# Kernel tuning notes

Measured on AMD Instinct MI355X. Metric: run time of the kernel, lower is better.

The kernel has to match this reference:

```python
import jax, jax.numpy as jnp
import numpy as np

NUM_ENT = 30000
NUM_ATTR_VALUES = 10000
NUM_NODES = NUM_ENT + NUM_ATTR_VALUES
NUM_REL = 230
NUM_ATTR_TYPES = 10
HIDDEN = 200          # num_bases=200 -> 1x1 block decomposition (per-rel diagonal)
N_EDGES = 600000
TIME_INTERVAL = 24
NUM_TIMESTAMPS = 365
PERIOD = 7
TRANX = 0.1
AMPY = 0.005
BATCH = 4096
RRELU_SLOPE = (1.0 / 8.0 + 1.0 / 3.0) / 2.0  # F.rrelu in eval mode


def setup_inputs() -> dict:
    key = jax.random.key(0)
    ks = jax.random.split(key, 12)
    ent_emb = jax.random.normal(ks[0], (NUM_ENT, HIDDEN), jnp.float32)            # nn.init.normal_
    attr_emb = jax.random.normal(ks[1], (NUM_ATTR_VALUES, HIDDEN), jnp.float32) * 0.05
    rel_emb = jax.random.normal(ks[2], (NUM_REL, HIDDEN), jnp.float32) * 0.1
    t = jnp.arange(NUM_TIMESTAMPS, dtype=jnp.float32)
    time_emb = (AMPY * (jnp.sin(2.0 * jnp.pi * t / PERIOD) + 1.0) + TRANX)[:, None]  # (T,1), frozen
    # RGCNBlockLayer weight: (num_rels, num_bases*submat_in*submat_out) = (10, 200)
    rgcn_weight = jax.random.normal(ks[3], (NUM_ATTR_TYPES, HIDDEN), jnp.float32) * 0.1
    dec_W = jax.random.normal(ks[4], (HIDDEN, 2 * HIDDEN + 1), jnp.float32) * 0.05
    dec_b = jnp.zeros((HIDDEN,), jnp.float32)
    edge_src = jax.random.randint(ks[5], (N_EDGES,), 0, NUM_NODES)
    edge_dst = jax.random.randint(ks[6], (N_EDGES,), 0, NUM_NODES)
    edge_type = jax.random.randint(ks[7], (N_EDGES,), 0, NUM_ATTR_TYPES)
    deg = jax.ops.segment_sum(jnp.ones((N_EDGES,), jnp.float32), edge_dst, num_segments=NUM_NODES)
    norm = (1.0 / jnp.clip(deg, 1.0))[:, None]  # (NUM_NODES, 1) in-degree norm
    ent_idx = jax.random.randint(ks[8], (BATCH,), 0, NUM_ENT)
    rel_idx = jax.random.randint(ks[9], (BATCH,), 0, NUM_REL)
    obj_idx = jax.random.randint(ks[10], (BATCH,), 0, NUM_ENT)
    time_raw = jax.random.randint(ks[11], (BATCH,), 0, NUM_TIMESTAMPS * TIME_INTERVAL)
    batch_data = jnp.stack([ent_idx, rel_idx, obj_idx, time_raw], axis=1)  # (B, 4)
    return {
        'ent_emb': ent_emb, 'attr_emb': attr_emb, 'rel_emb': rel_emb,
        'time_emb': time_emb, 'rgcn_weight': rgcn_weight,
        'dec_W': dec_W, 'dec_b': dec_b, 'norm': norm,
        'edge_src': edge_src, 'edge_dst': edge_dst, 'edge_type': edge_type,
        'batch_data': batch_data,
    }


def reference(ent_emb, attr_emb, rel_emb, time_emb, rgcn_weight, dec_W, dec_b,
              norm, edge_src, edge_dst, edge_type, batch_data):
    # --- RGCNBlockLayer (1x1 blocks): gather, per-relation diagonal multiply, scatter-sum ---
    h0 = jnp.concatenate([ent_emb, attr_emb], axis=0)           # (N, H)
    msg = h0[edge_src] * rgcn_weight[edge_type]                  # (E, H)
    agg = jax.ops.segment_sum(msg, edge_dst, num_segments=h0.shape[0])
    h = agg * norm                                               # apply_func: h * norm
    h = jnp.where(h >= 0, h, RRELU_SLOPE * h)                    # rrelu (eval); dropout=identity
    static_emb = h[:NUM_ENT]                                     # (num_ent, H)
    # --- embedding lookups ---
    ent = static_emb[batch_data[:, 0]]                           # (B, H)
    rel = rel_emb[batch_data[:, 1]]                              # (B, H)
    tim = time_emb[batch_data[:, 3] // TIME_INTERVAL]            # (B, 1)
    # --- decoder: tanh -> cat -> linear -> (dropout) -> relu -> mm ---
    x = jnp.concatenate([jnp.tanh(ent), rel, tim], axis=1)       # (B, 2H+1)
    x = x @ dec_W.T + dec_b                                      # (B, H)
    x = jax.nn.relu(x)
    return x @ static_emb.T                                      # (B, num_ent)
```

## Files before the change

### kernel.cpp

```cpp
#include <hip/hip_runtime.h>
#include <hip/hip_bf16.h>

#define NUM_ENT   30000
#define NUM_ATTR  10000
#define NUM_NODES 40000
#define NUM_TYPES 10
#define HIDDEN    200
#define KPAD      224
#define XP        416
#define NPAD      30080
#define N_EDGES   600000
#define BATCH     4096
#define XDIM      401
#define RRELU_SLOPE 0.22916666666666666f

using bf16x8 = __attribute__((ext_vector_type(8))) short;
using f32x4  = __attribute__((ext_vector_type(4))) float;
typedef __hip_bfloat16 bf16;

__device__ inline float bf2f(ushort u) { return __uint_as_float((unsigned)u << 16); }

__global__ void k_cvt(const float* __restrict__ ent, const float* __restrict__ attr,
                      ushort* __restrict__ h0b) {
    int i4 = blockIdx.x * blockDim.x + threadIdx.x;
    if (i4 >= NUM_NODES * HIDDEN / 4) return;
    int base = i4 * 4;
    const float* src = (base < NUM_ENT * HIDDEN) ? ent + base
                                                 : attr + (base - NUM_ENT * HIDDEN);
    float4 v = *reinterpret_cast<const float4*>(src);
    ushort4 o;
    o.x = __bfloat16_as_ushort(__float2bfloat16(v.x));
    o.y = __bfloat16_as_ushort(__float2bfloat16(v.y));
    o.z = __bfloat16_as_ushort(__float2bfloat16(v.z));
    o.w = __bfloat16_as_ushort(__float2bfloat16(v.w));
    *reinterpret_cast<ushort4*>(h0b + base) = o;
}

__global__ __launch_bounds__(1024) void k_prep(const float* __restrict__ norm,
                                               int* __restrict__ offsets,
                                               int* __restrict__ cursor) {
    __shared__ int part[1024];
    int t = threadIdx.x;
    const int CH = (NUM_ENT + 1023) / 1024;
    int base = t * CH;
    int caps[CH];
    int s = 0;
    for (int i = 0; i < CH; ++i) {
        int idx = base + i;
        int c = 0;
        if (idx < NUM_ENT) c = (int)(1.0f / norm[idx] + 0.5f);
        caps[i] = c;
        s += c;
    }
    part[t] = s;
    __syncthreads();
    for (int off = 1; off < 1024; off <<= 1) {
        int v = (t >= off) ? part[t - off] : 0;
        __syncthreads();
        part[t] += v;
        __syncthreads();
    }
    int run = (t == 0) ? 0 : part[t - 1];
    for (int i = 0; i < CH; ++i) {
        int idx = base + i;
        if (idx < NUM_ENT) {
            offsets[idx] = run;
            cursor[idx]  = run;
            run += caps[i];
        }
    }
}

__global__ void k_place(const int* __restrict__ edst, const int* __restrict__ esrc,
                        const int* __restrict__ etype, int* __restrict__ cursor,
                        int* __restrict__ sorted) {
    int e = blockIdx.x * blockDim.x + threadIdx.x;
    if (e < N_EDGES) {
        int d = edst[e];
        if (d < NUM_ENT) {
            int p = atomicAdd(&cursor[d], 1);
            sorted[p] = (esrc[e] << 4) | etype[e];
        }
    }
}

__global__ void k_aggregate(const ushort* __restrict__ h0b, const float* __restrict__ w,
                            const int* __restrict__ offsets, const int* __restrict__ cursor,
                            const int* __restrict__ sorted, const float* __restrict__ norm,
                            bf16* __restrict__ S) {
    __shared__ float wl[NUM_TYPES * HIDDEN];
    __shared__ float part[2][200];
    for (int i = threadIdx.x; i < NUM_TYPES * HIDDEN; i += blockDim.x)
        wl[i] = w[i];
    __syncthreads();

    int wid  = threadIdx.x >> 6;
    int lane = threadIdx.x & 63;
    int ln   = wid >> 1;
    int sub  = wid & 1;
    int n    = blockIdx.x * 2 + ln;
    bool live = (n < NUM_ENT);
    bool act  = lane < 50;
    int  c    = lane * 4;

    float4 a0 = make_float4(0, 0, 0, 0), a1 = a0, a2 = a0, a3 = a0;
    if (live) {
        int beg = offsets[n], end = cursor[n];
        int mid = beg + ((end - beg + 1) >> 1);
        int lo = sub ? mid : beg;
        int hi = sub ? end : mid;
        int e = lo;
        for (; e + 4 <= hi; e += 4) {
            int r0 = sorted[e + 0], r1 = sorted[e + 1], r2 = sorted[e + 2], r3 = sorted[e + 3];
            if (act) {
                ushort4 h0 = *reinterpret_cast<const ushort4*>(h0b + (size_t)(r0 >> 4) * HIDDEN + c);
                ushort4 h1 = *reinterpret_cast<const ushort4*>(h0b + (size_t)(r1 >> 4) * HIDDEN + c);
                ushort4 h2 = *reinterpret_cast<const ushort4*>(h0b + (size_t)(r2 >> 4) * HIDDEN + c);
                ushort4 h3 = *reinterpret_cast<const ushort4*>(h0b + (size_t)(r3 >> 4) * HIDDEN + c);
                const float* w0 = &wl[(r0 & 15) * HIDDEN + c];
                const float* w1 = &wl[(r1 & 15) * HIDDEN + c];
                const float* w2 = &wl[(r2 & 15) * HIDDEN + c];
                const float* w3 = &wl[(r3 & 15) * HIDDEN + c];
                a0.x += bf2f(h0.x) * w0[0]; a0.y += bf2f(h0.y) * w0[1];
                a0.z += bf2f(h0.z) * w0[2]; a0.w += bf2f(h0.w) * w0[3];
                a1.x += bf2f(h1.x) * w1[0]; a1.y += bf2f(h1.y) * w1[1];
                a1.z += bf2f(h1.z) * w1[2]; a1.w += bf2f(h1.w) * w1[3];
                a2.x += bf2f(h2.x) * w2[0]; a2.y += bf2f(h2.y) * w2[1];
                a2.z += bf2f(h2.z) * w2[2]; a2.w += bf2f(h2.w) * w2[3];
                a3.x += bf2f(h3.x) * w3[0]; a3.y += bf2f(h3.y) * w3[1];
                a3.z += bf2f(h3.z) * w3[2]; a3.w += bf2f(h3.w) * w3[3];
            }
        }
        for (; e < hi; ++e) {
            int r0 = sorted[e];
            if (act) {
                ushort4 h0 = *reinterpret_cast<const ushort4*>(h0b + (size_t)(r0 >> 4) * HIDDEN + c);
                const float* w0 = &wl[(r0 & 15) * HIDDEN + c];
                a0.x += bf2f(h0.x) * w0[0]; a0.y += bf2f(h0.y) * w0[1];
                a0.z += bf2f(h0.z) * w0[2]; a0.w += bf2f(h0.w) * w0[3];
            }
        }
    }
    float4 acc = make_float4(a0.x + a1.x + a2.x + a3.x,
                             a0.y + a1.y + a2.y + a3.y,
                             a0.z + a1.z + a2.z + a3.z,
                             a0.w + a1.w + a2.w + a3.w);
    if (live && sub == 1 && act)
        *reinterpret_cast<float4*>(&part[ln][c]) = acc;
    __syncthreads();

    if (sub == 0) {
        if (!live) {
            if (lane < KPAD / 4) {
                bf16 z4[4] = {};
                *reinterpret_cast<uint2*>(S + (size_t)n * KPAD + lane * 4) =
                    *reinterpret_cast<uint2*>(z4);
            }
        } else if (act) {
            float4 o = *reinterpret_cast<float4*>(&part[ln][c]);
            float nm = norm[n];
            float v0 = (acc.x + o.x) * nm;
            float v1 = (acc.y + o.y) * nm;
            float v2 = (acc.z + o.z) * nm;
            float v3 = (acc.w + o.w) * nm;
            v0 = (v0 >= 0.f) ? v0 : RRELU_SLOPE * v0;
            v1 = (v1 >= 0.f) ? v1 : RRELU_SLOPE * v1;
            v2 = (v2 >= 0.f) ? v2 : RRELU_SLOPE * v2;
            v3 = (v3 >= 0.f) ? v3 : RRELU_SLOPE * v3;
            bf16 t4[4] = {__float2bfloat16(v0), __float2bfloat16(v1),
                          __float2bfloat16(v2), __float2bfloat16(v3)};
            *reinterpret_cast<uint2*>(S + (size_t)n * KPAD + lane * 4) =
                *reinterpret_cast<uint2*>(t4);
        } else if (lane < KPAD / 4) {
            bf16 z4[4] = {};
            *reinterpret_cast<uint2*>(S + (size_t)n * KPAD + lane * 4) =
                *reinterpret_cast<uint2*>(z4);
        }
    }
}

__global__ void k_build_XW(const bf16* __restrict__ S, const float* __restrict__ rel_emb,
                           const float* __restrict__ time_emb, const float* __restrict__ dec_W,
                           const int* __restrict__ batch, bf16* __restrict__ X,
                           bf16* __restrict__ Wb) {
    int b = blockIdx.x;
    if (b < BATCH) {
        int m = b;
        int e  = batch[m * 4 + 0];
        int rl = batch[m * 4 + 1];
        int tr = batch[m * 4 + 3];
        float tv = time_emb[tr / 24];
        for (int c = threadIdx.x; c < XP; c += 256) {
            float v;
            if (c < HIDDEN) {
                v = tanhf(__bfloat162float(S[(size_t)e * KPAD + c]));
            } else if (c < 2 * HIDDEN) {
                v = rel_emb[(size_t)rl * HIDDEN + (c - HIDDEN)];
            } else if (c == 2 * HIDDEN) {
                v = tv;
            } else {
                v = 0.f;
            }
            X[(size_t)m * XP + c] = __float2bfloat16(v);
        }
    } else {
        int n = b - BATCH;
        for (int c = threadIdx.x; c < XP; c += 256) {
            float v = (n < HIDDEN && c < XDIM) ? dec_W[(size_t)n * XDIM + c] : 0.f;
            Wb[(size_t)n * XP + c] = __float2bfloat16(v);
        }
    }
}

__global__ __launch_bounds__(256) void k_dec_gemm(const bf16* __restrict__ Xb,
                                                  const bf16* __restrict__ Wbb,
                                                  const float* __restrict__ dec_b,
                                                  bf16* __restrict__ Y) {
    int wid  = threadIdx.x >> 6;
    int lane = threadIdx.x & 63;
    int row0 = blockIdx.x * 64 + wid * 16;
    int rsel = lane & 15;
    int koff = (lane >> 4) * 8;

    const short* Xp = reinterpret_cast<const short*>(Xb);
    const short* Wp = reinterpret_cast<const short*>(Wbb);

    f32x4 acc[14] = {};
#pragma unroll
    for (int kt = 0; kt < 13; ++kt) {
        int kbase = kt * 32 + koff;
        bf16x8 a = *reinterpret_cast<const bf16x8*>(Xp + (size_t)(row0 + rsel) * XP + kbase);
#pragma unroll
        for (int j = 0; j < 14; ++j) {
            bf16x8 b = *reinterpret_cast<const bf16x8*>(Wp + (size_t)(j * 16 + rsel) * XP + kbase);
            acc[j] = __builtin_amdgcn_mfma_f32_16x16x32_bf16(a, b, acc[j], 0, 0, 0);
        }
    }

    int crow = (lane >> 4) * 4;
    int ccol = lane & 15;
#pragma unroll
    for (int j = 0; j < 14; ++j) {
        int col = j * 16 + ccol;
        float bias = (col < HIDDEN) ? dec_b[col] : 0.f;
#pragma unroll
        for (int r = 0; r < 4; ++r) {
            int row = row0 + crow + r;
            float v = fmaxf(acc[j][r] + bias, 0.f);
            Y[(size_t)row * KPAD + col] = __float2bfloat16(v);
        }
    }
}

__global__ __launch_bounds__(256) void k_gemm(const bf16* __restrict__ Yb,
                                              const bf16* __restrict__ Sb,
                                              float* __restrict__ out) {
    __shared__ float eb[4][32 * 68];

    int bid = blockIdx.x;
    int xcd = bid & 7;
    int t   = (bid >> 3) + xcd * 940;
    int ytile = t & 31;
    int xtile = t >> 5;

    int wid  = threadIdx.x >> 6;
    int lane = threadIdx.x & 63;
    int wm = wid >> 1, wn = wid & 1;
    int row0 = ytile * 128 + wm * 64;
    int col0 = xtile * 128 + wn * 64;
    int rsel = lane & 15;
    int koff = (lane >> 4) * 8;

    const short* Yp = reinterpret_cast<const short*>(Yb);
    const short* Sp = reinterpret_cast<const short*>(Sb);

    f32x4 acc[4][4] = {};
#pragma unroll
    for (int kt = 0; kt < 7; ++kt) {
        int kbase = kt * 32 + koff;
        bf16x8 a[4], b[4];
#pragma unroll
        for (int i = 0; i < 4; ++i)
            a[i] = *reinterpret_cast<const bf16x8*>(Yp + (size_t)(row0 + i * 16 + rsel) * KPAD + kbase);
#pragma unroll
        for (int j = 0; j < 4; ++j)
            b[j] = *reinterpret_cast<const bf16x8*>(Sp + (size_t)(col0 + j * 16 + rsel) * KPAD + kbase);
#pragma unroll
        for (int i = 0; i < 4; ++i)
#pragma unroll
            for (int j = 0; j < 4; ++j)
                acc[i][j] = __builtin_amdgcn_mfma_f32_16x16x32_bf16(a[i], b[j], acc[i][j], 0, 0, 0);
    }

    float* myeb = eb[wid];
    int hi16 = lane >> 4;
    int lo16 = lane & 15;
#pragma unroll
    for (int h = 0; h < 2; ++h) {
        if (h) __syncthreads();
#pragma unroll
        for (int ii = 0; ii < 2; ++ii)
#pragma unroll
            for (int j = 0; j < 4; ++j)
#pragma unroll
                for (int r = 0; r < 4; ++r)
                    myeb[(ii * 16 + hi16 * 4 + r) * 68 + j * 16 + lo16] = acc[h * 2 + ii][j][r];
        __syncthreads();
#pragma unroll
        for (int q = 0; q < 8; ++q) {
            int lr = q * 4 + hi16;
            int lc = lo16 * 4;
            float4 v = *reinterpret_cast<float4*>(&myeb[lr * 68 + lc]);
            int grow = row0 + h * 32 + lr;
            int gcol = col0 + lc;
            if (gcol < NUM_ENT)
                *reinterpret_cast<float4*>(&out[(size_t)grow * NUM_ENT + gcol]) = v;
        }
    }
}

extern "C" void kernel_launch(void* const* d_in, const int* in_sizes, int n_in,
                              void* d_out, int out_size, void* d_ws, size_t ws_size,
                              hipStream_t stream) {
    const float* ent_emb  = (const float*)d_in[0];
    const float* attr_emb = (const float*)d_in[1];
    const float* rel_emb  = (const float*)d_in[2];
    const float* time_emb = (const float*)d_in[3];
    const float* rgcn_w   = (const float*)d_in[4];
    const float* dec_W    = (const float*)d_in[5];
    const float* dec_b    = (const float*)d_in[6];
    const float* norm     = (const float*)d_in[7];
    const int*   esrc     = (const int*)d_in[8];
    const int*   edst     = (const int*)d_in[9];
    const int*   etype    = (const int*)d_in[10];
    const int*   batch    = (const int*)d_in[11];

    char* ws = (char*)d_ws;
    bf16*   S      = (bf16*)ws;
    bf16*   Y      = (bf16*)(ws + 13475840);
    int*    offs   = (int*)(ws + 15310848);
    int*    cursor = (int*)(ws + 15430912);
    int*    sorted = (int*)(ws + 15550976);
    bf16*   X      = (bf16*)(ws + 18070976);
    bf16*   Wb     = (bf16*)(ws + 21478848);
    ushort* h0b    = (ushort*)(ws + 21665216);

    k_cvt  <<<(NUM_NODES * HIDDEN / 4 + 255) / 256, 256, 0, stream>>>(ent_emb, attr_emb, h0b);
    k_prep <<<1, 1024, 0, stream>>>(norm, offs, cursor);
    k_place<<<(N_EDGES + 255) / 256, 256, 0, stream>>>(edst, esrc, etype, cursor, sorted);
    k_aggregate<<<NPAD / 2, 256, 0, stream>>>(h0b, rgcn_w, offs, cursor, sorted, norm, S);
    k_build_XW<<<BATCH + KPAD, 256, 0, stream>>>(S, rel_emb, time_emb, dec_W, batch, X, Wb);
    k_dec_gemm<<<BATCH / 64, 256, 0, stream>>>(X, Wb, dec_b, Y);
    k_gemm<<<7520, 256, 0, stream>>>(Y, S, (float*)d_out);
}
```

Measured before the change: 400.8 us.

## Restructure output GEMM to persistent column panels with LDS-resident S tile

The final GEMM now launches one 512-thread block per 128-column panel of the entity matrix. Each block loads that panel's S slice into swizzled LDS once, then loops over all 4096 batch rows in 256-row chunks, streaming Y from global memory. The LDS-staged, float4-coalesced output store is replaced by direct scalar stores from the MFMA accumulator layout. Only 235 blocks run, which may underfill the GPU. The scalar stores are less coalesced on a write-bound 491 MB output.

```diff
diff --git a/kernel.cpp b/kernel.cpp
--- a/kernel.cpp
+++ b/kernel.cpp
@@ -252,69 +252,72 @@
     }
 }
 
-__global__ __launch_bounds__(256) void k_gemm(const bf16* __restrict__ Yb,
+__global__ __launch_bounds__(512) void k_gemm(const bf16* __restrict__ Yb,
                                               const bf16* __restrict__ Sb,
                                               float* __restrict__ out) {
-    __shared__ float eb[4][32 * 68];
-
-    int bid = blockIdx.x;
-    int xcd = bid & 7;
-    int t   = (bid >> 3) + xcd * 940;
-    int ytile = t & 31;
-    int xtile = t >> 5;
-
-    int wid  = threadIdx.x >> 6;
-    int lane = threadIdx.x & 63;
-    int wm = wid >> 1, wn = wid & 1;
-    int row0 = ytile * 128 + wm * 64;
-    int col0 = xtile * 128 + wn * 64;
+    __shared__ short Bs[128 * KPAD];
+
+    int panel = blockIdx.x;
+    int col0  = panel * 128;
+    int tid   = threadIdx.x;
+
+    {
+        const ushort* gB = (const ushort*)Sb + (size_t)col0 * KPAD;
+        char* Bb = (char*)Bs;
+#pragma unroll
+        for (int c = 0; c < 7; ++c) {
+            int chunk = tid + c * 512;
+            int row = chunk / 28;
+            int off = chunk - row * 28;
+            uint4 v = *reinterpret_cast<const uint4*>(gB + (size_t)row * KPAD + off * 8);
+            unsigned lb = (unsigned)(row * 448 + off * 16) ^ ((row & 7) << 4);
+            *reinterpret_cast<uint4*>(Bb + lb) = v;
+        }
+    }
+    __syncthreads();
+
+    int wid  = tid >> 6;
+    int lane = tid & 63;
     int rsel = lane & 15;
-    int koff = (lane >> 4) * 8;
-
-    const short* Yp = reinterpret_cast<const short*>(Yb);
-    const short* Sp = reinterpret_cast<const short*>(Sb);
-
-    f32x4 acc[4][4] = {};
-#pragma unroll
-    for (int kt = 0; kt < 7; ++kt) {
-        int kbase = kt * 32 + koff;
-        bf16x8 a[4], b[4];
-#pragma unroll
-        for (int i = 0; i < 4; ++i)
-            a[i] = *reinterpret_cast<const bf16x8*>(Yp + (size_t)(row0 + i * 16 + rsel) * KPAD + kbase);
-#pragma unroll
-        for (int j = 0; j < 4; ++j)
-            b[j] = *reinterpret_cast<const bf16x8*>(Sp + (size_t)(col0 + j * 16 + rsel) * KPAD + kbase);
-#pragma unroll
-        for (int i = 0; i < 4; ++i)
-#pragma unroll
-            for (int j = 0; j < 4; ++j)
-                acc[i][j] = __builtin_amdgcn_mfma_f32_16x16x32_bf16(a[i], b[j], acc[i][j], 0, 0, 0);
-    }
-
-    float* myeb = eb[wid];
-    int hi16 = lane >> 4;
-    int lo16 = lane & 15;
-#pragma unroll
-    for (int h = 0; h < 2; ++h) {
-        if (h) __syncthreads();
-#pragma unroll
-        for (int ii = 0; ii < 2; ++ii)
-#pragma unroll
-            for (int j = 0; j < 4; ++j)
-#pragma unroll
-                for (int r = 0; r < 4; ++r)
-                    myeb[(ii * 16 + hi16 * 4 + r) * 68 + j * 16 + lo16] = acc[h * 2 + ii][j][r];
-        __syncthreads();
-#pragma unroll
-        for (int q = 0; q < 8; ++q) {
-            int lr = q * 4 + hi16;
-            int lc = lo16 * 4;
-            float4 v = *reinterpret_cast<float4*>(&myeb[lr * 68 + lc]);
-            int grow = row0 + h * 32 + lr;
-            int gcol = col0 + lc;
-            if (gcol < NUM_ENT)
-                *reinterpret_cast<float4*>(&out[(size_t)grow * NUM_ENT + gcol]) = v;
+    int hi   = lane >> 4;
+    unsigned swr = (unsigned)(rsel & 7) << 4;
+    const char*  Bb = (const char*)Bs;
+    const short* Yp = (const short*)Yb;
+
+    int crow = hi * 4;
+    int ccol = lane & 15;
+
+    for (int mc = 0; mc < 16; ++mc) {
+        int rbase = mc * 256 + wid * 32;
+        f32x4 acc[2][8] = {};
+#pragma unroll
+        for (int kt = 0; kt < 7; ++kt) {
+            int ks = kt * 32 + hi * 8;
+            bf16x8 a[2];
+#pragma unroll
+            for (int i = 0; i < 2; ++i)
+                a[i] = *reinterpret_cast<const bf16x8*>(Yp + (size_t)(rbase + i * 16 + rsel) * KPAD + ks);
+#pragma unroll
+            for (int j = 0; j < 8; ++j) {
+                unsigned rb = (unsigned)((j * 16 + rsel) * 448 + kt * 64 + hi * 16);
+                bf16x8 b = *reinterpret_cast<const bf16x8*>(Bb + (rb ^ swr));
+#pragma unroll
+                for (int i = 0; i < 2; ++i)
+                    acc[i][j] = __builtin_amdgcn_mfma_f32_16x16x32_bf16(a[i], b, acc[i][j], 0, 0, 0);
+            }
+        }
+#pragma unroll
+        for (int j = 0; j < 8; ++j) {
+            int col = col0 + j * 16 + ccol;
+            if (col < NUM_ENT) {
+#pragma unroll
+                for (int i = 0; i < 2; ++i)
+#pragma unroll
+                    for (int r = 0; r < 4; ++r) {
+                        int row = rbase + i * 16 + crow + r;
+                        out[(size_t)row * NUM_ENT + col] = acc[i][j][r];
+                    }
+            }
         }
     }
 }
@@ -351,5 +354,5 @@
     k_aggregate<<<NPAD / 2, 256, 0, stream>>>(h0b, rgcn_w, offs, cursor, sorted, norm, S);
     k_build_XW<<<BATCH + KPAD, 256, 0, stream>>>(S, rel_emb, time_emb, dec_W, batch, X, Wb);
     k_dec_gemm<<<BATCH / 64, 256, 0, stream>>>(X, Wb, dec_b, Y);
-    k_gemm<<<7520, 256, 0, stream>>>(Y, S, (float*)d_out);
-}
+    k_gemm<<<235, 512, 0, stream>>>(Y, S, (float*)d_out);
+}
```

Result: slower. 428.2 us (+6.8%).
